# Kernel tuning notes

Hardware: AMD Instinct MI355X
Metric: run time of the kernel (lower is better)

## Reference

```python
import jax, jax.numpy as jnp
import numpy as np

H = 5  # hidden size
SEQ = 512
BATCH = 16384


def _lstm_layer(x, Wih, Whh, bih, bhh):
    # x: (B, S, D_in); weights follow PyTorch layout: W (4H, D), gate order i,f,g,o
    B = x.shape[0]
    b = bih + bhh
    xs = jnp.swapaxes(x, 0, 1)  # (S, B, D_in)
    # precompute input projections for all timesteps: (S, B, 4H)
    xproj = jnp.einsum('sbd,gd->sbg', xs, Wih) + b

    def step(carry, xp):
        h, c = carry
        gates = xp + h @ Whh.T  # (B, 4H)
        i, f, g, o = jnp.split(gates, 4, axis=-1)
        i = jax.nn.sigmoid(i)
        f = jax.nn.sigmoid(f)
        g = jnp.tanh(g)
        o = jax.nn.sigmoid(o)
        c = f * c + i * g
        h = o * jnp.tanh(c)
        return (h, c), h

    h0 = jnp.zeros((B, H), dtype=x.dtype)
    c0 = jnp.zeros((B, H), dtype=x.dtype)
    _, hs = jax.lax.scan(step, (h0, c0), xproj)  # hs: (S, B, H)
    return jnp.swapaxes(hs, 0, 1)  # (B, S, H)


def setup_inputs() -> dict:
    key = jax.random.key(0)
    ks = jax.random.split(key, 13)
    s = 1.0 / np.sqrt(H)
    u = lambda k, shp: jax.random.uniform(k, shp, jnp.float32, -s, s)
    return {
        'x': jax.random.normal(ks[0], (BATCH, SEQ, 1), jnp.float32),
        'Wih0': u(ks[1], (4 * H, 1)),
        'Whh0': u(ks[2], (4 * H, H)),
        'bih0': u(ks[3], (4 * H,)),
        'bhh0': u(ks[4], (4 * H,)),
        'Wih1': u(ks[5], (4 * H, H)),
        'Whh1': u(ks[6], (4 * H, H)),
        'bih1': u(ks[7], (4 * H,)),
        'bhh1': u(ks[8], (4 * H,)),
        'W1': jax.random.uniform(ks[9], (512, SEQ * H), jnp.float32, -1 / np.sqrt(SEQ * H), 1 / np.sqrt(SEQ * H)),
        'b1': jax.random.uniform(ks[10], (512,), jnp.float32, -1 / np.sqrt(SEQ * H), 1 / np.sqrt(SEQ * H)),
        'W2': jax.random.uniform(ks[11], (1, 512), jnp.float32, -1 / np.sqrt(512), 1 / np.sqrt(512)),
        'b2': jax.random.uniform(ks[12], (1,), jnp.float32, -1 / np.sqrt(512), 1 / np.sqrt(512)),
    }


def reference(x, Wih0, Whh0, bih0, bhh0, Wih1, Whh1, bih1, bhh1, W1, b1, W2, b2):
    h = _lstm_layer(x, Wih0, Whh0, bih0, bhh0)   # (B, S, 5)
    h = _lstm_layer(h, Wih1, Whh1, bih1, bhh1)   # (B, S, 5)
    h = h.reshape(h.shape[0], -1)                # (B, S*5)
    h = h @ W1.T + b1                            # (B, 512)
    out = h @ W2.T + b2                          # (B, 1)
    return out
```

## Files before the change

kernel.cpp:

```cpp
#include <hip/hip_runtime.h>

#define BATCH 16384
#define SEQ 512

typedef float f4 __attribute__((ext_vector_type(4)));
typedef _Float16 half8 __attribute__((ext_vector_type(8)));

#define SIGS (-1.44269504088896f)
#define TNHS (-2.88539008177793f)

union HB { unsigned int u[4]; half8 h; };

__device__ __forceinline__ float bpermf(int addr, float v) {
    return __int_as_float(__builtin_amdgcn_ds_bpermute(addr, __float_as_int(v)));
}
__device__ __forceinline__ unsigned int bpermu(int addr, unsigned int v) {
    return (unsigned int)__builtin_amdgcn_ds_bpermute(addr, (int)v);
}
__device__ __forceinline__ unsigned int h16(float v) {
    return (unsigned int)__builtin_bit_cast(unsigned short, (_Float16)v);
}
__device__ __forceinline__ unsigned int lolo(unsigned int a, unsigned int b) {
    return __builtin_amdgcn_perm(b, a, 0x05040100u);
}
__device__ __forceinline__ unsigned int lohi(unsigned int a, unsigned int b) {
    return __builtin_amdgcn_perm(b, a, 0x07060100u);
}
__device__ __forceinline__ unsigned int hilo(unsigned int a, unsigned int b) {
    return __builtin_amdgcn_perm(b, a, 0x05040302u);
}

__device__ __forceinline__ float act1(float Pi, float Pf, float Pg, float Po, float& c) {
    float A = __builtin_amdgcn_exp2f(Pi);
    float F = __builtin_amdgcn_exp2f(Pf);
    float B = __builtin_amdgcn_exp2f(Pg);
    float O = __builtin_amdgcn_exp2f(Po);
    float ab = (1.0f + A) * (1.0f + B);
    float f1 = 1.0f + F;
    float r  = __builtin_amdgcn_rcpf(ab * f1);
    float f  = ab * r;
    float ig = (1.0f - B) * (f1 * r);
    c = fmaf(f, c, ig);
    float pc = fminf(c * TNHS, 60.0f);
    float Ce = __builtin_amdgcn_exp2f(pc);
    float rho = __builtin_amdgcn_rcpf((1.0f + O) * (1.0f + Ce));
    return (1.0f - Ce) * rho;
}

__global__ __launch_bounds__(256) void collapse_kernel(
    const float* __restrict__ W1, const float* __restrict__ b1,
    const float* __restrict__ W2, const float* __restrict__ b2,
    float* __restrict__ ws)
{
    const int kl = threadIdx.x & 15;
    const int ms = threadIdx.x >> 4;
    const int k  = blockIdx.x * 16 + kl;
    const float* w1p = W1 + (size_t)(ms * 32) * 2560 + k;
    const float* w2p = W2 + ms * 32;
    float acc = 0.f;
    #pragma unroll 8
    for (int m = 0; m < 32; ++m) acc = fmaf(w2p[m], w1p[(size_t)m * 2560], acc);
    __shared__ float red[16][17];
    red[ms][kl] = acc;
    __syncthreads();
    if (ms == 0) {
        float s = 0.f;
        #pragma unroll
        for (int r = 0; r < 16; ++r) s += red[r][kl];
        const int t = k / 5, u = k % 5;
        if (u < 4) ws[8 * t + 2 * u] = s;
        else { ws[8*t + 1] = s; ws[8*t + 3] = s; ws[8*t + 5] = s; ws[8*t + 7] = s; }
    }
    if (blockIdx.x == 0) {
        const int t = threadIdx.x;
        float p = fmaf(W2[t], b1[t], W2[t + 256] * b1[t + 256]);
        #pragma unroll
        for (int off = 32; off > 0; off >>= 1) p += __shfl_down(p, off);
        __shared__ float cred[4];
        if ((t & 63) == 0) cred[t >> 6] = p;
        __syncthreads();
        if (t == 0) ws[4096] = cred[0] + cred[1] + cred[2] + cred[3] + b2[0];
    }
}

__global__ __launch_bounds__(64)
__attribute__((amdgpu_waves_per_eu(1, 1)))
void lstm_fused_kernel(
    const float* __restrict__ x,
    const float* __restrict__ Wih0, const float* __restrict__ Whh0,
    const float* __restrict__ bih0, const float* __restrict__ bhh0,
    const float* __restrict__ Wih1, const float* __restrict__ Whh1,
    const float* __restrict__ bih1, const float* __restrict__ bhh1,
    const float* __restrict__ ws, float* __restrict__ out)
{
    const int lane = threadIdx.x;
    const int e15  = lane & 15;
    const int g    = lane >> 4;
    const int e    = blockIdx.x * 16 + e15;
    const float sc[4] = {SIGS, SIGS, TNHS, SIGS};

    HB aL0a, aL0b, aL1a, aL1b;
    {
        const int m = e15, kb = g * 8;
        {
            const int u = m >> 2, gi = m & 3, row = gi * 5 + u;
            float w[8];
            #pragma unroll
            for (int j = 0; j < 8; ++j) {
                const int k = kb + j;
                float v = (k == 0) ? Wih0[row] : (k <= 5 ? Whh0[row * 5 + k - 1] : 0.f);
                w[j] = v * sc[gi];
            }
            #pragma unroll
            for (int d = 0; d < 4; ++d) aL0a.u[d] = h16(w[2*d]) | (h16(w[2*d+1]) << 16);
        }
        {
            float w[8] = {0,0,0,0,0,0,0,0};
            if (m >= 4 && m < 8) {
                const int gi = m - 4, row = gi * 5 + 4;
                #pragma unroll
                for (int j = 0; j < 8; ++j) {
                    const int k = kb + j;
                    float v = (k == 0) ? Wih0[row] : (k <= 5 ? Whh0[row * 5 + k - 1] : 0.f);
                    w[j] = v * sc[gi];
                }
            }
            #pragma unroll
            for (int d = 0; d < 4; ++d) aL0b.u[d] = h16(w[2*d]) | (h16(w[2*d+1]) << 16);
        }
        {
            const int u = m >> 2, gi = m & 3, row = gi * 5 + u;
            float w[8];
            #pragma unroll
            for (int j = 0; j < 8; ++j) {
                const int k = kb + j;
                float v = (k <= 4) ? Wih1[row * 5 + k]
                        : (k <= 9 ? Whh1[row * 5 + k - 5] : 0.f);
                w[j] = v * sc[gi];
            }
            #pragma unroll
            for (int d = 0; d < 4; ++d) aL1a.u[d] = h16(w[2*d]) | (h16(w[2*d+1]) << 16);
        }
        {
            float w[8] = {0,0,0,0,0,0,0,0};
            if (m >= 8 && m < 12) {
                const int gi = m - 8, row = gi * 5 + 4;
                #pragma unroll
                for (int j = 0; j < 8; ++j) {
                    const int k = kb + j;
                    float v = (k <= 4) ? Wih1[row * 5 + k]
                            : (k <= 9 ? Whh1[row * 5 + k - 5] : 0.f);
                    w[j] = v * sc[gi];
                }
            }
            #pragma unroll
            for (int d = 0; d < 4; ++d) aL1b.u[d] = h16(w[2*d]) | (h16(w[2*d+1]) << 16);
        }
    }
    f4 cL0a, cL1a, cb;
    #pragma unroll
    for (int r = 0; r < 4; ++r) {
        cL0a[r] = (bih0[r*5+g] + bhh0[r*5+g]) * sc[r];
        cL1a[r] = (bih1[r*5+g] + bhh1[r*5+g]) * sc[r];
        cb[r]   = (g == 1) ? (bih0[r*5+4] + bhh0[r*5+4]) * sc[r]
                : (g == 2) ? (bih1[r*5+4] + bhh1[r*5+4]) * sc[r] : 0.f;
    }

    const float* xp = x + (size_t)e * SEQ;
    const bool l16 = lane < 16;
    const int aP1 = (e15 + 16) << 2, aP2 = (e15 + 32) << 2, aP3 = (e15 + 48) << 2;
    const int aP5 = ((l16 ? lane + 16 : lane + 32) & 63) << 2;

    float c0 = 0.f, c1 = 0.f, c4 = 0.f, acc = 0.f, acc4 = 0.f;
    f4 dA, dC, dD;

    {
        HB B0, B1;
        B0.u[0] = h16(xp[0]);  B0.u[1] = B0.u[2] = B0.u[3] = 0u;
        dA = __builtin_amdgcn_mfma_f32_16x16x32_f16(aL0a.h, B0.h, cL0a, 0, 0, 0);
        f4 dBD = __builtin_amdgcn_mfma_f32_16x16x32_f16(aL0b.h, B0.h, cb, 0, 0, 0);
        float hA0 = act1(dA[0], dA[1], dA[2], dA[3], c0);
        float h40 = act1(dBD[0], dBD[1], dBD[2], dBD[3], c4);
        if (g == 2) { h40 = 0.f; c4 = 0.f; }
        unsigned hx0 = h16(hA0) | (h16(h40) << 16);
        unsigned q1 = bpermu(aP1, hx0), q2 = bpermu(aP2, hx0), q3 = bpermu(aP3, hx0);
        B0.u[0] = lolo(h16(xp[1]), hx0);
        B0.u[1] = lolo(q1, q2);
        B0.u[2] = lohi(q3, q1);
        B0.u[3] = 0u;
        dA = __builtin_amdgcn_mfma_f32_16x16x32_f16(aL0a.h, B0.h, cL0a, 0, 0, 0);
        f4 nBD = __builtin_amdgcn_mfma_f32_16x16x32_f16(aL0b.h, B0.h, cb, 0, 0, 0);
        B1.u[0] = l16 ? lolo(hx0, q1) : lohi(0u, q2);
        B1.u[1] = lolo(q2, q3);
        B1.u[2] = hilo(q1, 0u);
        B1.u[3] = 0u;
        dC = __builtin_amdgcn_mfma_f32_16x16x32_f16(aL1a.h, B1.h, cL1a, 0, 0, 0);
        dD = __builtin_amdgcn_mfma_f32_16x16x32_f16(aL1b.h, B1.h, nBD, 0, 0, 0);
    }

    unsigned xh16[4]; float wM[4], w4b[4];
    #pragma unroll
    for (int u = 0; u < 4; ++u) {
        xh16[u] = h16(xp[2 + u]);
        float2 w = *(const float2*)(ws + 8 * u + 2 * g);
        wM[u] = w.x;  w4b[u] = w.y;
    }

    auto body = [&](unsigned xh_next, float wMu, float w4u) {
        float hAn = act1(dA[0], dA[1], dA[2], dA[3], c0);
        float h4n = act1(dD[0], dD[1], dD[2], dD[3], c4);
        unsigned hx0 = h16(hAn) | (h16(h4n) << 16);
        unsigned q1 = bpermu(aP1, hx0);
        unsigned q2 = bpermu(aP2, hx0);
        unsigned q3 = bpermu(aP3, hx0);
        float hCn = act1(dC[0], dC[1], dC[2], dC[3], c1);
        acc  = fmaf(hCn, wMu, acc);
        acc4 = fmaf(h4n, w4u, acc4);
        unsigned hc16 = h16(hCn);
        unsigned ra = bpermu(aP5, hc16);
        unsigned rb = bpermu(aP2, hc16);
        HB B0;
        B0.u[0] = lolo(xh_next, hx0);
        B0.u[1] = lolo(q1, q2);
        B0.u[2] = lohi(q3, q1);
        B0.u[3] = 0u;
        f4 nA  = __builtin_amdgcn_mfma_f32_16x16x32_f16(aL0a.h, B0.h, cL0a, 0, 0, 0);
        f4 nBD = __builtin_amdgcn_mfma_f32_16x16x32_f16(aL0b.h, B0.h, cb, 0, 0, 0);
        HB B1;
        B1.u[0] = l16 ? lolo(hx0, q1)
                      : lohi(ra, q2);
        B1.u[1] = lolo(q2, q3);
        B1.u[2] = hilo(q1, hc16);
        B1.u[3] = lolo(ra, rb);
        dC = __builtin_amdgcn_mfma_f32_16x16x32_f16(aL1a.h, B1.h, cL1a, 0, 0, 0);
        dD = __builtin_amdgcn_mfma_f32_16x16x32_f16(aL1b.h, B1.h, nBD, 0, 0, 0);
        dA = nA;
    };

    for (int m = 1; m < 513; m += 4) {
        unsigned xhn[4]; float wMn[4], w4n[4];
        #pragma unroll
        for (int u = 0; u < 4; ++u) {
            xhn[u] = h16(xp[min(m + 5 + u, SEQ - 1)]);
            const int t = min(m + 3 + u, SEQ - 1);
            float2 w = *(const float2*)(ws + 8 * t + 2 * g);
            wMn[u] = w.x;  w4n[u] = w.y;
        }
        #pragma unroll
        for (int u = 0; u < 4; ++u) body(xh16[u], wM[u], w4b[u]);
        #pragma unroll
        for (int u = 0; u < 4; ++u) { xh16[u] = xhn[u]; wM[u] = wMn[u]; w4b[u] = w4n[u]; }
    }

    float accT = acc + ((g == 2) ? acc4 : 0.f);
    float t0 = bpermf(e15 << 2, accT);
    float t1 = bpermf((e15 + 16) << 2, accT);
    float t2 = bpermf((e15 + 32) << 2, accT);
    float t3 = bpermf((e15 + 48) << 2, accT);
    if (lane < 16) out[e] = (t0 + t1) + (t2 + t3) + ws[4096];
}

extern "C" void kernel_launch(void* const* d_in, const int* in_sizes, int n_in,
                              void* d_out, int out_size, void* d_ws, size_t ws_size,
                              hipStream_t stream) {
    const float* x    = (const float*)d_in[0];
    const float* Wih0 = (const float*)d_in[1];
    const float* Whh0 = (const float*)d_in[2];
    const float* bih0 = (const float*)d_in[3];
    const float* bhh0 = (const float*)d_in[4];
    const float* Wih1 = (const float*)d_in[5];
    const float* Whh1 = (const float*)d_in[6];
    const float* bih1 = (const float*)d_in[7];
    const float* bhh1 = (const float*)d_in[8];
    const float* W1   = (const float*)d_in[9];
    const float* b1   = (const float*)d_in[10];
    const float* W2   = (const float*)d_in[11];
    const float* b2   = (const float*)d_in[12];
    float* out = (float*)d_out;
    float* ws  = (float*)d_ws;

    collapse_kernel<<<160, 256, 0, stream>>>(W1, b1, W2, b2, ws);
    lstm_fused_kernel<<<BATCH / 16, 64, 0, stream>>>(x, Wih0, Whh0, bih0, bhh0,
                                                     Wih1, Whh1, bih1, bhh1, ws, out);
}
```

Baseline: 237.5 us.

## Use 16x16x16 MFMA with K-lane layout to eliminate bpermute exchanges

Switches the recurrent gate matmuls from the 16x16x32 MFMA to the 16x16x16 variant. The K dimension is laid out so each lane group supplies its own hidden unit's values, so the per-step ds_bpermute shuffles of hidden state are no longer needed. Merges the three per-step LSTM activations into one routine that shares reciprocals across cells through product tricks, and tightens the tanh clamp. This shortens the serial per-timestep dependency chain, at the cost of extra multiplies and a smaller fp32 range margin in the shared reciprocal.

```diff
diff --git a/kernel.cpp b/kernel.cpp
--- a/kernel.cpp
+++ b/kernel.cpp
@@ -4,47 +4,59 @@
 #define SEQ 512
 
 typedef float f4 __attribute__((ext_vector_type(4)));
-typedef _Float16 half8 __attribute__((ext_vector_type(8)));
+typedef _Float16 half4 __attribute__((ext_vector_type(4)));
 
 #define SIGS (-1.44269504088896f)
 #define TNHS (-2.88539008177793f)
 
-union HB { unsigned int u[4]; half8 h; };
+union HB2 { unsigned int u[2]; half4 h; };
 
 __device__ __forceinline__ float bpermf(int addr, float v) {
     return __int_as_float(__builtin_amdgcn_ds_bpermute(addr, __float_as_int(v)));
 }
-__device__ __forceinline__ unsigned int bpermu(int addr, unsigned int v) {
-    return (unsigned int)__builtin_amdgcn_ds_bpermute(addr, (int)v);
-}
 __device__ __forceinline__ unsigned int h16(float v) {
     return (unsigned int)__builtin_bit_cast(unsigned short, (_Float16)v);
 }
 __device__ __forceinline__ unsigned int lolo(unsigned int a, unsigned int b) {
     return __builtin_amdgcn_perm(b, a, 0x05040100u);
 }
-__device__ __forceinline__ unsigned int lohi(unsigned int a, unsigned int b) {
-    return __builtin_amdgcn_perm(b, a, 0x07060100u);
-}
-__device__ __forceinline__ unsigned int hilo(unsigned int a, unsigned int b) {
-    return __builtin_amdgcn_perm(b, a, 0x05040302u);
-}
-
-__device__ __forceinline__ float act1(float Pi, float Pf, float Pg, float Po, float& c) {
-    float A = __builtin_amdgcn_exp2f(Pi);
-    float F = __builtin_amdgcn_exp2f(Pf);
-    float B = __builtin_amdgcn_exp2f(Pg);
-    float O = __builtin_amdgcn_exp2f(Po);
-    float ab = (1.0f + A) * (1.0f + B);
-    float f1 = 1.0f + F;
-    float r  = __builtin_amdgcn_rcpf(ab * f1);
-    float f  = ab * r;
-    float ig = (1.0f - B) * (f1 * r);
-    c = fmaf(f, c, ig);
-    float pc = fminf(c * TNHS, 60.0f);
-    float Ce = __builtin_amdgcn_exp2f(pc);
-    float rho = __builtin_amdgcn_rcpf((1.0f + O) * (1.0f + Ce));
-    return (1.0f - Ce) * rho;
+
+__device__ __forceinline__ void act3(const f4& dA, const f4& dD, const f4& dC,
+                                     float& c0, float& c4, float& c1,
+                                     float& hA, float& h4, float& hC) {
+    float A0 = __builtin_amdgcn_exp2f(dA[0]), F0 = __builtin_amdgcn_exp2f(dA[1]);
+    float B0 = __builtin_amdgcn_exp2f(dA[2]), O0 = __builtin_amdgcn_exp2f(dA[3]);
+    float A1 = __builtin_amdgcn_exp2f(dD[0]), F1 = __builtin_amdgcn_exp2f(dD[1]);
+    float B1 = __builtin_amdgcn_exp2f(dD[2]), O1 = __builtin_amdgcn_exp2f(dD[3]);
+    float A2 = __builtin_amdgcn_exp2f(dC[0]), F2 = __builtin_amdgcn_exp2f(dC[1]);
+    float B2 = __builtin_amdgcn_exp2f(dC[2]), O2 = __builtin_amdgcn_exp2f(dC[3]);
+
+    float t0 = 1.0f + A0, t1 = 1.0f + A1, t2 = 1.0f + A2;
+    float ab0 = fmaf(t0, B0, t0), ab1 = fmaf(t1, B1, t1), ab2 = fmaf(t2, B2, t2);
+    float D0 = fmaf(ab0, F0, ab0), D1 = fmaf(ab1, F1, ab1), D2 = fmaf(ab2, F2, ab2);
+    float p01 = D0 * D1, p12 = D1 * D2, p02 = D0 * D2;
+    float r = __builtin_amdgcn_rcpf(p01 * D2);
+    float r0 = r * p12, r1 = r * p02, r2 = r * p01;
+
+    float bm0 = 1.0f - B0, bm1 = 1.0f - B1, bm2 = 1.0f - B2;
+    float w0 = fmaf(bm0, F0, bm0), w1 = fmaf(bm1, F1, bm1), w2 = fmaf(bm2, F2, bm2);
+    c0 = fmaf(ab0 * r0, c0, w0 * r0);
+    c4 = fmaf(ab1 * r1, c4, w1 * r1);
+    c1 = fmaf(ab2 * r2, c1, w2 * r2);
+
+    float pc0 = fminf(c0 * TNHS, 17.0f);
+    float pc1 = fminf(c4 * TNHS, 17.0f);
+    float pc2 = fminf(c1 * TNHS, 17.0f);
+    float Ce0 = __builtin_amdgcn_exp2f(pc0);
+    float Ce1 = __builtin_amdgcn_exp2f(pc1);
+    float Ce2 = __builtin_amdgcn_exp2f(pc2);
+    float o0 = 1.0f + O0, o1 = 1.0f + O1, o2 = 1.0f + O2;
+    float e0 = fmaf(o0, Ce0, o0), e1 = fmaf(o1, Ce1, o1), e2 = fmaf(o2, Ce2, o2);
+    float q01 = e0 * e1, q12 = e1 * e2, q02 = e0 * e2;
+    float rr = __builtin_amdgcn_rcpf(q01 * e2);
+    hA = (1.0f - Ce0) * (rr * q12);
+    h4 = (1.0f - Ce1) * (rr * q02);
+    hC = (1.0f - Ce2) * (rr * q01);
 }
 
 __global__ __launch_bounds__(256) void collapse_kernel(
@@ -99,62 +111,48 @@
     const int e    = blockIdx.x * 16 + e15;
     const float sc[4] = {SIGS, SIGS, TNHS, SIGS};
 
-    HB aL0a, aL0b, aL1a, aL1b;
+    HB2 aL0a, aL0b, aL1a, aL1b;
     {
-        const int m = e15, kb = g * 8;
-        {
-            const int u = m >> 2, gi = m & 3, row = gi * 5 + u;
-            float w[8];
-            #pragma unroll
-            for (int j = 0; j < 8; ++j) {
-                const int k = kb + j;
-                float v = (k == 0) ? Wih0[row] : (k <= 5 ? Whh0[row * 5 + k - 1] : 0.f);
-                w[j] = v * sc[gi];
+        const int m = e15;
+        {
+            const int u = m >> 2, gi = m & 3, gr = gi * 5 + u;
+            const float s = sc[gi];
+            float w0 = Whh0[gr * 5 + g];
+            float w1 = (g == 0) ? Wih0[gr] : (g == 1 ? Whh0[gr * 5 + 4] : 0.f);
+            aL0a.u[0] = h16(w0 * s) | (h16(w1 * s) << 16);
+            aL0a.u[1] = 0u;
+        }
+        {
+            float w0 = 0.f, w1 = 0.f, s = 0.f;
+            if (m >= 4 && m < 8) {
+                const int gi = m - 4, gr = gi * 5 + 4;
+                s = sc[gi];
+                w0 = Whh0[gr * 5 + g];
+                w1 = (g == 0) ? Wih0[gr] : (g == 1 ? Whh0[gr * 5 + 4] : 0.f);
             }
-            #pragma unroll
-            for (int d = 0; d < 4; ++d) aL0a.u[d] = h16(w[2*d]) | (h16(w[2*d+1]) << 16);
-        }
-        {
-            float w[8] = {0,0,0,0,0,0,0,0};
-            if (m >= 4 && m < 8) {
-                const int gi = m - 4, row = gi * 5 + 4;
-                #pragma unroll
-                for (int j = 0; j < 8; ++j) {
-                    const int k = kb + j;
-                    float v = (k == 0) ? Wih0[row] : (k <= 5 ? Whh0[row * 5 + k - 1] : 0.f);
-                    w[j] = v * sc[gi];
-                }
+            aL0b.u[0] = h16(w0 * s) | (h16(w1 * s) << 16);
+            aL0b.u[1] = 0u;
+        }
+        {
+            const int u = m >> 2, gi = m & 3, gr = gi * 5 + u;
+            const float s = sc[gi];
+            float w0 = Wih1[gr * 5 + g];
+            float w1 = Whh1[gr * 5 + g];
+            float w2 = (g == 1) ? Wih1[gr * 5 + 4] : (g == 2 ? Whh1[gr * 5 + 4] : 0.f);
+            aL1a.u[0] = h16(w0 * s) | (h16(w1 * s) << 16);
+            aL1a.u[1] = h16(w2 * s);
+        }
+        {
+            float w0 = 0.f, w1 = 0.f, w2 = 0.f, s = 0.f;
+            if (m >= 8 && m < 12) {
+                const int gi = m - 8, gr = gi * 5 + 4;
+                s = sc[gi];
+                w0 = Wih1[gr * 5 + g];
+                w1 = Whh1[gr * 5 + g];
+                w2 = (g == 1) ? Wih1[gr * 5 + 4] : (g == 2 ? Whh1[gr * 5 + 4] : 0.f);
             }
-            #pragma unroll
-            for (int d = 0; d < 4; ++d) aL0b.u[d] = h16(w[2*d]) | (h16(w[2*d+1]) << 16);
-        }
-        {
-            const int u = m >> 2, gi = m & 3, row = gi * 5 + u;
-            float w[8];
-            #pragma unroll
-            for (int j = 0; j < 8; ++j) {
-                const int k = kb + j;
-                float v = (k <= 4) ? Wih1[row * 5 + k]
-                        : (k <= 9 ? Whh1[row * 5 + k - 5] : 0.f);
-                w[j] = v * sc[gi];
-            }
-            #pragma unroll
-            for (int d = 0; d < 4; ++d) aL1a.u[d] = h16(w[2*d]) | (h16(w[2*d+1]) << 16);
-        }
-        {
-            float w[8] = {0,0,0,0,0,0,0,0};
-            if (m >= 8 && m < 12) {
-                const int gi = m - 8, row = gi * 5 + 4;
-                #pragma unroll
-                for (int j = 0; j < 8; ++j) {
-                    const int k = kb + j;
-                    float v = (k <= 4) ? Wih1[row * 5 + k]
-                            : (k <= 9 ? Whh1[row * 5 + k - 5] : 0.f);
-                    w[j] = v * sc[gi];
-                }
-            }
-            #pragma unroll
-            for (int d = 0; d < 4; ++d) aL1b.u[d] = h16(w[2*d]) | (h16(w[2*d+1]) << 16);
+            aL1b.u[0] = h16(w0 * s) | (h16(w1 * s) << 16);
+            aL1b.u[1] = h16(w2 * s);
         }
     }
     f4 cL0a, cL1a, cb;
@@ -167,35 +165,31 @@
     }
 
     const float* xp = x + (size_t)e * SEQ;
-    const bool l16 = lane < 16;
-    const int aP1 = (e15 + 16) << 2, aP2 = (e15 + 32) << 2, aP3 = (e15 + 48) << 2;
-    const int aP5 = ((l16 ? lane + 16 : lane + 32) & 63) << 2;
+    const bool isg0 = (g == 0), isg2 = (g == 2);
 
     float c0 = 0.f, c1 = 0.f, c4 = 0.f, acc = 0.f, acc4 = 0.f;
     f4 dA, dC, dD;
 
     {
-        HB B0, B1;
-        B0.u[0] = h16(xp[0]);  B0.u[1] = B0.u[2] = B0.u[3] = 0u;
-        dA = __builtin_amdgcn_mfma_f32_16x16x32_f16(aL0a.h, B0.h, cL0a, 0, 0, 0);
-        f4 dBD = __builtin_amdgcn_mfma_f32_16x16x32_f16(aL0b.h, B0.h, cb, 0, 0, 0);
-        float hA0 = act1(dA[0], dA[1], dA[2], dA[3], c0);
-        float h40 = act1(dBD[0], dBD[1], dBD[2], dBD[3], c4);
-        if (g == 2) { h40 = 0.f; c4 = 0.f; }
-        unsigned hx0 = h16(hA0) | (h16(h40) << 16);
-        unsigned q1 = bpermu(aP1, hx0), q2 = bpermu(aP2, hx0), q3 = bpermu(aP3, hx0);
-        B0.u[0] = lolo(h16(xp[1]), hx0);
-        B0.u[1] = lolo(q1, q2);
-        B0.u[2] = lohi(q3, q1);
-        B0.u[3] = 0u;
-        dA = __builtin_amdgcn_mfma_f32_16x16x32_f16(aL0a.h, B0.h, cL0a, 0, 0, 0);
-        f4 nBD = __builtin_amdgcn_mfma_f32_16x16x32_f16(aL0b.h, B0.h, cb, 0, 0, 0);
-        B1.u[0] = l16 ? lolo(hx0, q1) : lohi(0u, q2);
-        B1.u[1] = lolo(q2, q3);
-        B1.u[2] = hilo(q1, 0u);
-        B1.u[3] = 0u;
-        dC = __builtin_amdgcn_mfma_f32_16x16x32_f16(aL1a.h, B1.h, cL1a, 0, 0, 0);
-        dD = __builtin_amdgcn_mfma_f32_16x16x32_f16(aL1b.h, B1.h, nBD, 0, 0, 0);
+        unsigned xh0 = h16(xp[0]);
+        HB2 b0; b0.u[0] = isg0 ? (xh0 << 16) : 0u; b0.u[1] = 0u;
+        dA = __builtin_amdgcn_mfma_f32_16x16x16f16(aL0a.h, b0.h, cL0a, 0, 0, 0);
+        f4 dBD = __builtin_amdgcn_mfma_f32_16x16x16f16(aL0b.h, b0.h, cb, 0, 0, 0);
+        dC = cL1a;
+        dD = dBD;
+        float hA, h4, hC;
+        act3(dA, dD, dC, c0, c4, c1, hA, h4, hC);
+        if (isg2) { h4 = 0.f; c4 = 0.f; }
+        hC = 0.f; c1 = 0.f;
+        unsigned hx0 = h16(hA) | (h16(h4) << 16);
+        unsigned xh1 = h16(xp[1]);
+        HB2 B0n, B1n;
+        B0n.u[0] = isg0 ? lolo(hx0, xh1) : hx0;  B0n.u[1] = 0u;
+        B1n.u[0] = hx0 & 0xFFFFu;                B1n.u[1] = hx0 >> 16;
+        dA = __builtin_amdgcn_mfma_f32_16x16x16f16(aL0a.h, B0n.h, cL0a, 0, 0, 0);
+        f4 nBD = __builtin_amdgcn_mfma_f32_16x16x16f16(aL0b.h, B0n.h, cb, 0, 0, 0);
+        dC = __builtin_amdgcn_mfma_f32_16x16x16f16(aL1a.h, B1n.h, cL1a, 0, 0, 0);
+        dD = __builtin_amdgcn_mfma_f32_16x16x16f16(aL1b.h, B1n.h, nBD, 0, 0, 0);
     }
 
     unsigned xh16[4]; float wM[4], w4b[4];
@@ -207,34 +201,19 @@
     }
 
     auto body = [&](unsigned xh_next, float wMu, float w4u) {
-        float hAn = act1(dA[0], dA[1], dA[2], dA[3], c0);
-        float h4n = act1(dD[0], dD[1], dD[2], dD[3], c4);
-        unsigned hx0 = h16(hAn) | (h16(h4n) << 16);
-        unsigned q1 = bpermu(aP1, hx0);
-        unsigned q2 = bpermu(aP2, hx0);
-        unsigned q3 = bpermu(aP3, hx0);
-        float hCn = act1(dC[0], dC[1], dC[2], dC[3], c1);
-        acc  = fmaf(hCn, wMu, acc);
-        acc4 = fmaf(h4n, w4u, acc4);
-        unsigned hc16 = h16(hCn);
-        unsigned ra = bpermu(aP5, hc16);
-        unsigned rb = bpermu(aP2, hc16);
-        HB B0;
-        B0.u[0] = lolo(xh_next, hx0);
-        B0.u[1] = lolo(q1, q2);
-        B0.u[2] = lohi(q3, q1);
-        B0.u[3] = 0u;
-        f4 nA  = __builtin_amdgcn_mfma_f32_16x16x32_f16(aL0a.h, B0.h, cL0a, 0, 0, 0);
-        f4 nBD = __builtin_amdgcn_mfma_f32_16x16x32_f16(aL0b.h, B0.h, cb, 0, 0, 0);
-        HB B1;
-        B1.u[0] = l16 ? lolo(hx0, q1)
-                      : lohi(ra, q2);
-        B1.u[1] = lolo(q2, q3);
-        B1.u[2] = hilo(q1, hc16);
-        B1.u[3] = lolo(ra, rb);
-        dC = __builtin_amdgcn_mfma_f32_16x16x32_f16(aL1a.h, B1.h, cL1a, 0, 0, 0);
-        dD = __builtin_amdgcn_mfma_f32_16x16x32_f16(aL1b.h, B1.h, nBD, 0, 0, 0);
-        dA = nA;
+        float hA, h4, hC;
+        act3(dA, dD, dC, c0, c4, c1, hA, h4, hC);
+        acc  = fmaf(hC, wMu, acc);
+        acc4 = fmaf(h4, w4u, acc4);
+        unsigned hx0  = h16(hA) | (h16(h4) << 16);
+        unsigned hc16 = h16(hC);
+        HB2 B0n, B1n;
+        B0n.u[0] = isg0 ? lolo(hx0, xh_next) : hx0;  B0n.u[1] = 0u;
+        B1n.u[0] = lolo(hx0, hc16);                  B1n.u[1] = hx0 >> 16;
+        dA = __builtin_amdgcn_mfma_f32_16x16x16f16(aL0a.h, B0n.h, cL0a, 0, 0, 0);
+        f4 nBD = __builtin_amdgcn_mfma_f32_16x16x16f16(aL0b.h, B0n.h, cb, 0, 0, 0);
+        dC = __builtin_amdgcn_mfma_f32_16x16x16f16(aL1a.h, B1n.h, cL1a, 0, 0, 0);
+        dD = __builtin_amdgcn_mfma_f32_16x16x16f16(aL1b.h, B1n.h, nBD, 0, 0, 0);
     };
 
     for (int m = 1; m < 513; m += 4) {
@@ -252,7 +231,7 @@
         for (int u = 0; u < 4; ++u) { xh16[u] = xhn[u]; wM[u] = wMn[u]; w4b[u] = w4n[u]; }
     }
 
-    float accT = acc + ((g == 2) ? acc4 : 0.f);
+    float accT = acc + (isg2 ? acc4 : 0.f);
     float t0 = bpermf(e15 << 2, accT);
     float t1 = bpermf((e15 + 16) << 2, accT);
     float t2 = bpermf((e15 + 32) << 2, accT);
```

Result: faster. 212.6 us (-10.5%).
